# Kernel tuning notes

Measured on AMD Instinct MI355X. Metric: run time of the kernel, lower is better.

The kernel has to match this reference:

```python
import jax, jax.numpy as jnp
import numpy as np

LN_EPS = 1e-5  # standard LayerNorm eps
OPM_EPS = 1e-3  # module's eps for the mean denominator


def layer_norm(x, g, b):
    mu = jnp.mean(x, axis=-1, keepdims=True)
    var = jnp.mean((x - mu) ** 2, axis=-1, keepdims=True)
    return (x - mu) * jax.lax.rsqrt(var + LN_EPS) * g + b


def setup_inputs() -> dict:
    key = jax.random.key(0)
    ks = jax.random.split(key, 6)
    N, L1, K, L2 = 1, 256, 128, 1024
    c_s, c_m, c_z, ch = 384, 256, 128, 32
    return {
        "s": jax.random.normal(ks[0], (N, L1, c_s), jnp.float32),
        "m": jax.random.normal(ks[1], (N, K, L2, c_m), jnp.float32),
        "ln_ab_g": jnp.ones((c_s,), jnp.float32),
        "ln_ab_b": jnp.zeros((c_s,), jnp.float32),
        "ln_ag_g": jnp.ones((c_m,), jnp.float32),
        "ln_ag_b": jnp.zeros((c_m,), jnp.float32),
        "W_ab": jax.random.normal(ks[2], (c_s, ch), jnp.float32) * 0.02,
        "b_ab": jnp.zeros((ch,), jnp.float32),
        "W_ag": jax.random.normal(ks[3], (c_m, ch), jnp.float32) * 0.02,
        "b_ag": jnp.zeros((ch,), jnp.float32),
        "W_out": jax.random.normal(ks[4], (ch * ch, c_z), jnp.float32) * 0.02,
        "b_out": jnp.zeros((c_z,), jnp.float32),
    }


def reference(s, m, ln_ab_g, ln_ab_b, ln_ag_g, ln_ag_b,
              W_ab, b_ab, W_ag, b_ag, W_out, b_out):
    # s: [N, L1, c_s], m: [N, K, L2, c_m]
    K = m.shape[1]
    ch = W_ab.shape[-1]
    c_z = W_out.shape[-1]

    a = layer_norm(s, ln_ab_g, ln_ab_b) @ W_ab + b_ab          # [N, L1, ch]
    mm = layer_norm(m, ln_ag_g, ln_ag_b) @ W_ag + b_ag          # [N, K, L2, ch]

    # In the original, `a` is repeated along K before the einsum, so it is
    # K-invariant and sum_k a[i,c] * m[k,j,e] == a[i,c] * (sum_k m[k,j,e]).
    m_sum = jnp.sum(mm, axis=1)                                  # [N, L2, ch]

    # outer[n,i,j,c,e] -> flatten (c,e) with c outer -> linear_out
    Wo = W_out.reshape(ch, ch, c_z)                              # [c, e, z]
    z = jnp.einsum('nic,nje,cez->nijz', a, m_sum, Wo) + b_out    # [N, L1, L2, c_z]

    # norm = sum over K of ones == K, plus eps
    return z / (jnp.float32(K) + OPM_EPS)
```

## Files before the change

kernel.cpp:

```cpp
#include <hip/hip_runtime.h>

#define L1V 256
#define L2V 1024
#define KV  128
#define CSV 384
#define CMV 256
#define CHV 32
#define CZV 128

__device__ __forceinline__ float4 f4zero() { return make_float4(0.f,0.f,0.f,0.f); }

__device__ __forceinline__ void ln_accum(const float4 x, float4& xs) {
  float s1 = x.x + x.y + x.z + x.w;
  float s2 = fmaf(x.x, x.x, fmaf(x.y, x.y, fmaf(x.z, x.z, x.w * x.w)));
  #pragma unroll
  for (int off = 32; off > 0; off >>= 1) {
    s1 += __shfl_xor(s1, off, 64);
    s2 += __shfl_xor(s2, off, 64);
  }
  const float mu   = s1 * (1.0f / CMV);
  const float rstd = rsqrtf(s2 * (1.0f / CMV) - mu * mu + 1e-5f);
  xs.x = fmaf(x.x - mu, rstd, xs.x);
  xs.y = fmaf(x.y - mu, rstd, xs.y);
  xs.z = fmaf(x.z - mu, rstd, xs.z);
  xs.w = fmaf(x.w - mu, rstd, xs.w);
}

__global__ __launch_bounds__(256) void msum_kernel(
    const float* __restrict__ m, const float* __restrict__ g,
    const float* __restrict__ b, const float* __restrict__ Wag,
    const float* __restrict__ bag, float* __restrict__ msum)
{
  const int j    = blockIdx.x;
  const int tid  = threadIdx.x;
  const int wave = tid >> 6;
  const int lane = tid & 63;

  const float4* base = (const float4*)m;

  float4 xs = f4zero();
  float4 x0 = base[(((size_t)wave << 10) + j) * 64 + lane];
  float4 x1 = base[(((size_t)(wave + 4) << 10) + j) * 64 + lane];

  for (int k = wave; k < KV; k += 8) {
    float4 n0 = f4zero(), n1 = f4zero();
    if (k + 8  < KV) n0 = base[(((size_t)(k + 8)  << 10) + j) * 64 + lane];
    if (k + 12 < KV) n1 = base[(((size_t)(k + 12) << 10) + j) * 64 + lane];
    ln_accum(x0, xs);
    ln_accum(x1, xs);
    x0 = n0; x1 = n1;
  }

  __shared__ float xsum[4][CMV];
  ((float4*)xsum[wave])[lane] = xs;
  __syncthreads();

  __shared__ float y[CMV];
  y[tid] = (xsum[0][tid] + xsum[1][tid] + xsum[2][tid] + xsum[3][tid]) * g[tid]
           + (float)KV * b[tid];
  __syncthreads();

  const int c     = tid & 31;
  const int chunk = tid >> 5;
  float p = 0.f;
  #pragma unroll
  for (int q = 0; q < 32; ++q) {
    const int e = (chunk << 5) + q;
    p = fmaf(y[e], Wag[(e << 5) + c], p);
  }
  __shared__ float pr[256];
  pr[tid] = p;
  __syncthreads();
  if (tid < 32) {
    float acc = 0.f;
    #pragma unroll
    for (int r = 0; r < 8; ++r) acc += pr[tid + (r << 5)];
    msum[(j << 5) + tid] = acc + (float)KV * bag[tid];
  }
}

__global__ __launch_bounds__(384) void a_kernel(
    const float* __restrict__ s, const float* __restrict__ g,
    const float* __restrict__ b, const float* __restrict__ Wab,
    const float* __restrict__ bab, float* __restrict__ a)
{
  const int i    = blockIdx.x;
  const int tid  = threadIdx.x;
  const int wave = tid >> 6;
  const int lane = tid & 63;

  const float x = s[i * CSV + tid];
  float s1 = x, s2 = x * x;
  #pragma unroll
  for (int off = 32; off > 0; off >>= 1) {
    s1 += __shfl_xor(s1, off, 64);
    s2 += __shfl_xor(s2, off, 64);
  }
  __shared__ float r1[6], r2[6];
  if (lane == 0) { r1[wave] = s1; r2[wave] = s2; }
  __syncthreads();
  float t1 = 0.f, t2 = 0.f;
  #pragma unroll
  for (int w = 0; w < 6; ++w) { t1 += r1[w]; t2 += r2[w]; }
  const float mu   = t1 * (1.0f / CSV);
  const float rstd = rsqrtf(t2 * (1.0f / CSV) - mu * mu + 1e-5f);

  __shared__ float y[CSV];
  y[tid] = (x - mu) * rstd * g[tid] + b[tid];
  __syncthreads();

  const int c     = tid & 31;
  const int chunk = tid >> 5;
  float p = 0.f;
  #pragma unroll
  for (int q = 0; q < 32; ++q) {
    const int e = (chunk << 5) + q;
    p = fmaf(y[e], Wab[(e << 5) + c], p);
  }
  __shared__ float pr[CSV];
  pr[tid] = p;
  __syncthreads();
  if (tid < 32) {
    float acc = 0.f;
    #pragma unroll
    for (int r = 0; r < 12; ++r) acc += pr[tid + (r << 5)];
    a[(i << 5) + tid] = acc + bab[tid];
  }
}

__global__ __launch_bounds__(256) void t_kernel(
    const float* __restrict__ a, const float* __restrict__ Wout,
    float* __restrict__ T)
{
  const int tid = threadIdx.x;
  const int idx = (blockIdx.x << 8) + tid;
  const int i0  = blockIdx.y << 4;

  __shared__ float as[16 * 32];
  #pragma unroll
  for (int r = 0; r < 2; ++r) {
    const int t = (r << 8) + tid;
    as[t] = a[(i0 << 5) + t];
  }
  __syncthreads();

  float w[32];
  #pragma unroll
  for (int c = 0; c < 32; ++c) w[c] = Wout[(c << 12) + idx];

  #pragma unroll 4
  for (int ii = 0; ii < 16; ++ii) {
    float acc = 0.f;
    #pragma unroll
    for (int c = 0; c < 32; ++c)
      acc = fmaf(as[(ii << 5) + c], w[c], acc);
    T[((size_t)(i0 + ii) << 12) + idx] = acc;
  }
}

__global__ __launch_bounds__(256) void out_kernel(
    const float* __restrict__ msum, const float* __restrict__ T,
    const float* __restrict__ bout, float* __restrict__ out)
{
  const int half = blockIdx.x;
  const int i    = blockIdx.y;
  const int tid  = threadIdx.x;
  const int zq   = (tid & 31) << 2;
  const int jg   = tid >> 5;

  float4 Treg[32];
  #pragma unroll
  for (int e = 0; e < 32; ++e)
    Treg[e] = *(const float4*)(T + ((size_t)i << 12) + (e << 7) + zq);

  const float4 bz = *(const float4*)(bout + zq);
  const float inv_norm = 1.0f / ((float)KV + 1e-3f);

  __shared__ float ms[64 * CHV];

  for (int tile = 0; tile < 8; ++tile) {
    const int j0 = (half << 9) + (tile << 6);
    __syncthreads();
    ((float4*)ms)[tid]       = ((const float4*)(msum + ((size_t)j0 << 5)))[tid];
    ((float4*)ms)[tid + 256] = ((const float4*)(msum + ((size_t)j0 << 5)))[tid + 256];
    __syncthreads();

    #pragma unroll
    for (int jj = 0; jj < 8; ++jj) {
      const int j = jg + (jj << 3);
      const float4* mr = (const float4*)(ms + (j << 5));
      float4 acc = f4zero();
      #pragma unroll
      for (int eq = 0; eq < 8; ++eq) {
        const float4 m4 = mr[eq];
        const float4 t0 = Treg[(eq << 2) + 0];
        const float4 t1 = Treg[(eq << 2) + 1];
        const float4 t2 = Treg[(eq << 2) + 2];
        const float4 t3 = Treg[(eq << 2) + 3];
        acc.x = fmaf(m4.x, t0.x, fmaf(m4.y, t1.x, fmaf(m4.z, t2.x, fmaf(m4.w, t3.x, acc.x))));
        acc.y = fmaf(m4.x, t0.y, fmaf(m4.y, t1.y, fmaf(m4.z, t2.y, fmaf(m4.w, t3.y, acc.y))));
        acc.z = fmaf(m4.x, t0.z, fmaf(m4.y, t1.z, fmaf(m4.z, t2.z, fmaf(m4.w, t3.z, acc.z))));
        acc.w = fmaf(m4.x, t0.w, fmaf(m4.y, t1.w, fmaf(m4.z, t2.w, fmaf(m4.w, t3.w, acc.w))));
      }
      float4 o;
      o.x = (acc.x + bz.x) * inv_norm;
      o.y = (acc.y + bz.y) * inv_norm;
      o.z = (acc.z + bz.z) * inv_norm;
      o.w = (acc.w + bz.w) * inv_norm;
      *(float4*)(out + ((size_t)i << 17) + ((size_t)(j0 + j) << 7) + zq) = o;
    }
  }
}

extern "C" void kernel_launch(void* const* d_in, const int* in_sizes, int n_in,
                              void* d_out, int out_size, void* d_ws, size_t ws_size,
                              hipStream_t stream) {
  (void)in_sizes; (void)n_in; (void)out_size; (void)ws_size;
  const float* s    = (const float*)d_in[0];
  const float* m    = (const float*)d_in[1];
  const float* g_ab = (const float*)d_in[2];
  const float* b_ab = (const float*)d_in[3];
  const float* g_ag = (const float*)d_in[4];
  const float* b_ag = (const float*)d_in[5];
  const float* Wab  = (const float*)d_in[6];
  const float* bab  = (const float*)d_in[7];
  const float* Wag  = (const float*)d_in[8];
  const float* bag  = (const float*)d_in[9];
  const float* Wout = (const float*)d_in[10];
  const float* bout = (const float*)d_in[11];
  float* out = (float*)d_out;

  float* msum = (float*)d_ws;
  float* a    = msum + 32768;
  float* T    = a + 8192;

  hipLaunchKernelGGL(msum_kernel, dim3(1024), dim3(256), 0, stream,
                     m, g_ag, b_ag, Wag, bag, msum);
  hipLaunchKernelGGL(a_kernel, dim3(256), dim3(384), 0, stream,
                     s, g_ab, b_ab, Wab, bab, a);
  hipLaunchKernelGGL(t_kernel, dim3(16, 16), dim3(256), 0, stream,
                     a, Wout, T);
  hipLaunchKernelGGL(out_kernel, dim3(2, 256), dim3(256), 0, stream,
                     msum, T, bout, out);
}
```

Baseline: 282.7 us.

## Restructure output kernel to wave-uniform msum rows and use nontemporal loads/stores

The output kernel no longer stages msum tiles in shared memory with block barriers. Each wave now owns 128 consecutive j rows, reads msum rows with wave-uniform (scalar-broadcast) loads double-buffered in registers, and each lane computes two z outputs with inv_norm folded into T and the bias. Output writes and the streaming reads of m in the msum kernel use nontemporal hints to reduce cache pollution. The trade-off is narrower float2 stores and less FMA work per msum load, which could lower store efficiency or arithmetic intensity.

```diff
diff --git a/kernel.cpp b/kernel.cpp
--- a/kernel.cpp
+++ b/kernel.cpp
@@ -8,7 +8,15 @@
 #define CHV 32
 #define CZV 128
 
+typedef float f4v __attribute__((ext_vector_type(4)));
+typedef float f2v __attribute__((ext_vector_type(2)));
+
 __device__ __forceinline__ float4 f4zero() { return make_float4(0.f,0.f,0.f,0.f); }
+
+__device__ __forceinline__ float4 nt_load4(const float4* p) {
+  f4v t = __builtin_nontemporal_load((const f4v*)p);
+  return make_float4(t.x, t.y, t.z, t.w);
+}
 
 __device__ __forceinline__ void ln_accum(const float4 x, float4& xs) {
   float s1 = x.x + x.y + x.z + x.w;
@@ -39,13 +47,13 @@
   const float4* base = (const float4*)m;
 
   float4 xs = f4zero();
-  float4 x0 = base[(((size_t)wave << 10) + j) * 64 + lane];
-  float4 x1 = base[(((size_t)(wave + 4) << 10) + j) * 64 + lane];
+  float4 x0 = nt_load4(&base[(((size_t)wave << 10) + j) * 64 + lane]);
+  float4 x1 = nt_load4(&base[(((size_t)(wave + 4) << 10) + j) * 64 + lane]);
 
   for (int k = wave; k < KV; k += 8) {
     float4 n0 = f4zero(), n1 = f4zero();
-    if (k + 8  < KV) n0 = base[(((size_t)(k + 8)  << 10) + j) * 64 + lane];
-    if (k + 12 < KV) n1 = base[(((size_t)(k + 12) << 10) + j) * 64 + lane];
+    if (k + 8  < KV) n0 = nt_load4(&base[(((size_t)(k + 8)  << 10) + j) * 64 + lane]);
+    if (k + 12 < KV) n1 = nt_load4(&base[(((size_t)(k + 12) << 10) + j) * 64 + lane]);
     ln_accum(x0, xs);
     ln_accum(x1, xs);
     x0 = n0; x1 = n1;
@@ -164,52 +172,56 @@
 {
   const int half = blockIdx.x;
   const int i    = blockIdx.y;
-  const int tid  = threadIdx.x;
-  const int zq   = (tid & 31) << 2;
-  const int jg   = tid >> 5;
-
-  float4 Treg[32];
-  #pragma unroll
-  for (int e = 0; e < 32; ++e)
-    Treg[e] = *(const float4*)(T + ((size_t)i << 12) + (e << 7) + zq);
-
-  const float4 bz = *(const float4*)(bout + zq);
+  const int wid  = __builtin_amdgcn_readfirstlane((int)(threadIdx.x >> 6));
+  const int lane = threadIdx.x & 63;
+  const int z0   = lane << 1;
+
   const float inv_norm = 1.0f / ((float)KV + 1e-3f);
 
-  __shared__ float ms[64 * CHV];
-
-  for (int tile = 0; tile < 8; ++tile) {
-    const int j0 = (half << 9) + (tile << 6);
-    __syncthreads();
-    ((float4*)ms)[tid]       = ((const float4*)(msum + ((size_t)j0 << 5)))[tid];
-    ((float4*)ms)[tid + 256] = ((const float4*)(msum + ((size_t)j0 << 5)))[tid + 256];
-    __syncthreads();
-
-    #pragma unroll
-    for (int jj = 0; jj < 8; ++jj) {
-      const int j = jg + (jj << 3);
-      const float4* mr = (const float4*)(ms + (j << 5));
-      float4 acc = f4zero();
-      #pragma unroll
-      for (int eq = 0; eq < 8; ++eq) {
-        const float4 m4 = mr[eq];
-        const float4 t0 = Treg[(eq << 2) + 0];
-        const float4 t1 = Treg[(eq << 2) + 1];
-        const float4 t2 = Treg[(eq << 2) + 2];
-        const float4 t3 = Treg[(eq << 2) + 3];
-        acc.x = fmaf(m4.x, t0.x, fmaf(m4.y, t1.x, fmaf(m4.z, t2.x, fmaf(m4.w, t3.x, acc.x))));
-        acc.y = fmaf(m4.x, t0.y, fmaf(m4.y, t1.y, fmaf(m4.z, t2.y, fmaf(m4.w, t3.y, acc.y))));
-        acc.z = fmaf(m4.x, t0.z, fmaf(m4.y, t1.z, fmaf(m4.z, t2.z, fmaf(m4.w, t3.z, acc.z))));
-        acc.w = fmaf(m4.x, t0.w, fmaf(m4.y, t1.w, fmaf(m4.z, t2.w, fmaf(m4.w, t3.w, acc.w))));
-      }
-      float4 o;
-      o.x = (acc.x + bz.x) * inv_norm;
-      o.y = (acc.y + bz.y) * inv_norm;
-      o.z = (acc.z + bz.z) * inv_norm;
-      o.w = (acc.w + bz.w) * inv_norm;
-      *(float4*)(out + ((size_t)i << 17) + ((size_t)(j0 + j) << 7) + zq) = o;
-    }
-  }
+  float2 Tr[32];
+  #pragma unroll
+  for (int e = 0; e < 32; ++e) {
+    const float2 t = *(const float2*)(T + ((size_t)i << 12) + (e << 7) + z0);
+    Tr[e] = make_float2(t.x * inv_norm, t.y * inv_norm);
+  }
+  float2 bz = *(const float2*)(bout + z0);
+  bz.x *= inv_norm; bz.y *= inv_norm;
+
+  const int j0 = (half << 9) + (wid << 7);
+  float* const outp = out + ((size_t)i << 17);
+
+  float4 mA[8], mB[8];
+
+#define LOADROW(BUF, J) do {                                                \
+    const float4* mr = (const float4*)(msum + ((size_t)(J) << 5));          \
+    _Pragma("unroll")                                                       \
+    for (int q = 0; q < 8; ++q) BUF[q] = mr[q];                             \
+  } while (0)
+
+#define FMA_STORE(BUF, J) do {                                              \
+    float ax = bz.x, ay = bz.y;                                             \
+    _Pragma("unroll")                                                       \
+    for (int q = 0; q < 8; ++q) {                                           \
+      const float4 mq = BUF[q];                                             \
+      ax = fmaf(mq.x, Tr[(q<<2)+0].x, ax); ay = fmaf(mq.x, Tr[(q<<2)+0].y, ay); \
+      ax = fmaf(mq.y, Tr[(q<<2)+1].x, ax); ay = fmaf(mq.y, Tr[(q<<2)+1].y, ay); \
+      ax = fmaf(mq.z, Tr[(q<<2)+2].x, ax); ay = fmaf(mq.z, Tr[(q<<2)+2].y, ay); \
+      ax = fmaf(mq.w, Tr[(q<<2)+3].x, ax); ay = fmaf(mq.w, Tr[(q<<2)+3].y, ay); \
+    }                                                                       \
+    f2v ov; ov.x = ax; ov.y = ay;                                           \
+    __builtin_nontemporal_store(ov,                                         \
+        (f2v*)(outp + ((size_t)(J) << 7) + z0));                            \
+  } while (0)
+
+  LOADROW(mA, j0);
+  for (int jj = 0; jj < 128; jj += 2) {
+    LOADROW(mB, j0 + jj + 1);
+    FMA_STORE(mA, j0 + jj);
+    if (jj + 2 < 128) LOADROW(mA, j0 + jj + 2);
+    FMA_STORE(mB, j0 + jj + 1);
+  }
+#undef LOADROW
+#undef FMA_STORE
 }
 
 extern "C" void kernel_launch(void* const* d_in, const int* in_sizes, int n_in,
```

Result: faster. 269.8 us, median of 2 (-4.6%).
